# Optimization experiments

Hardware: AMD Instinct MI355X
Metric: run time of the kernel (lower is better)

Reference implementation:

```python
import jax, jax.numpy as jnp
import numpy as np

N_NODES = 50000
N_EDGES = 640000
DIMS = [128, 256, 128]


def setup_inputs() -> dict:
    key = jax.random.key(0)
    ks = jax.random.split(key, 8)
    x = jax.random.normal(ks[0], (N_NODES, DIMS[0]), dtype=jnp.float32)
    src = jax.random.randint(ks[1], (N_EDGES,), 0, N_NODES)
    dst = jax.random.randint(ks[2], (N_EDGES,), 0, N_NODES)
    # ensure no pre-existing self loops so add_remaining_self_loops == append all loops
    dst = jnp.where(dst == src, (dst + 1) % N_NODES, dst)
    edge_index = jnp.stack([src, dst]).astype(jnp.int64)
    # SAGEConv lin_l weights (root_weight=False -> only neighbor linear), Kaiming-ish init
    def lin(k, fan_in, fan_out):
        s = 1.0 / np.sqrt(fan_in)
        kw, kb = jax.random.split(k)
        W = jax.random.uniform(kw, (fan_out, fan_in), minval=-s, maxval=s, dtype=jnp.float32)
        b = jax.random.uniform(kb, (fan_out,), minval=-s, maxval=s, dtype=jnp.float32)
        return W, b
    W1, b1 = lin(ks[3], DIMS[0], DIMS[1])
    W2, b2 = lin(ks[4], DIMS[1], DIMS[2])
    logit_scale = jnp.asarray(np.log(1.0 / 0.07), dtype=jnp.float32)
    return {"x": x, "edge_index": edge_index, "W1": W1, "b1": b1,
            "W2": W2, "b2": b2, "logit_scale": logit_scale}


def reference(x, edge_index, W1, b1, W2, b2, logit_scale):
    N = x.shape[0]
    loops = jnp.arange(N, dtype=edge_index.dtype)
    src = jnp.concatenate([edge_index[0], loops])  # add_remaining_self_loops
    dst = jnp.concatenate([edge_index[1], loops])
    deg = jax.ops.segment_sum(jnp.ones_like(dst, dtype=x.dtype), dst, num_segments=N)
    inv_deg = 1.0 / deg  # deg >= 1 thanks to self loops

    def sage_conv(y, W, b):
        # mean aggregation of source features at destination, then linear
        agg = jax.ops.segment_sum(y[src], dst, num_segments=N) * inv_deg[:, None]
        return agg @ W.T + b

    y = jax.nn.relu(sage_conv(x, W1, b1))
    y = sage_conv(y, W2, b2)
    # F.normalize(p=2, dim=-1, eps=1e-12)
    nrm = jnp.maximum(jnp.linalg.norm(y, axis=-1, keepdims=True), 1e-12)
    y = y / nrm
    return y * jnp.exp(logit_scale)
```

## Files before the change

kernel.cpp:

```cpp
#include <hip/hip_runtime.h>
#include <hip/hip_bf16.h>

#define N_NODES 50000
#define NPAD 50048
#define ZROW N_NODES
#define D0 128
#define D1 256
#define D2 128
#define N4 1600000
#define NB4 1601536
#define CAP 64
#define PREP_BLOCKS 2048

typedef __attribute__((ext_vector_type(8))) short short8;
typedef __attribute__((ext_vector_type(8))) unsigned short ushort8;
typedef __attribute__((ext_vector_type(4))) float f32x4;

static __device__ __forceinline__ unsigned short f2bf(float f) {
    __hip_bfloat16 h = __float2bfloat16(f);
    return *(unsigned short*)&h;
}
static __device__ __forceinline__ float bf2f(unsigned short u) {
    return __uint_as_float(((unsigned int)u) << 16);
}

__global__ __launch_bounds__(256) void k_prep(const float* __restrict__ x,
                                              unsigned short* __restrict__ x_bf,
                                              const float* __restrict__ W1,
                                              const float* __restrict__ W2,
                                              unsigned short* __restrict__ W1p,
                                              unsigned short* __restrict__ W2p,
                                              const int* __restrict__ ei,
                                              int* __restrict__ cursor,
                                              unsigned short* __restrict__ csr, int E) {
    __shared__ int s_is64;
    if (threadIdx.x < 64) {
        int lane = threadIdx.x;
        int nz = 0;
#pragma unroll
        for (int k = 0; k < 4; k++) nz += (ei[2 * (lane * 4 + k) + 1] != 0);
#pragma unroll
        for (int off = 32; off > 0; off >>= 1) nz += __shfl_down(nz, off, 64);
        if (lane == 0) s_is64 = (nz == 0) ? 1 : 0;
    }
    __syncthreads();
    const int NT = PREP_BLOCKS * 256;
    int tid0 = blockIdx.x * 256 + threadIdx.x;

    int npairs = (E + 1) / 2;
    if (tid0 < npairs) {
        int p = tid0;
        int is64 = s_is64;
        int es0, ed0, es1, ed1;
        if (is64) {
            int4 sp = ((const int4*)ei)[p];
            int4 dp = ((const int4*)(ei + 2 * (size_t)E))[p];
            es0 = sp.x; es1 = sp.z; ed0 = dp.x; ed1 = dp.z;
        } else {
            int2 sp = ((const int2*)ei)[p];
            int2 dp = ((const int2*)(ei + (size_t)E))[p];
            es0 = sp.x; es1 = sp.y; ed0 = dp.x; ed1 = dp.y;
        }
        int p0 = atomicAdd(&cursor[ed0], 1);
        if (p0 < CAP) csr[(size_t)ed0 * CAP + p0] = (unsigned short)es0;
        if (2 * p + 1 < E) {
            int p1 = atomicAdd(&cursor[ed1], 1);
            if (p1 < CAP) csr[(size_t)ed1 * CAP + p1] = (unsigned short)es1;
        }
    }

    for (int i = tid0; i < NB4; i += NT) {
        if (i < N4) {
            float4 v = ((const float4*)x)[i];
            ushort4 u;
            u.x = f2bf(v.x); u.y = f2bf(v.y); u.z = f2bf(v.z); u.w = f2bf(v.w);
            ((ushort4*)x_bf)[i] = u;
        } else {
            ushort4 z = {0, 0, 0, 0};
            ((ushort4*)x_bf)[i] = z;
        }
    }

    if (tid0 < 2 * D0 * D1) {
        int idx = tid0;
        if (idx < D0 * D1) {
            int j = idx & 7, lane = (idx >> 3) & 63, tile = idx >> 9;
            int ct = tile & 15, kt = tile >> 4;
            int k = kt * 32 + (lane >> 4) * 8 + j;
            int n = ct * 16 + (lane & 15);
            W1p[idx] = f2bf(W1[n * D0 + k]);
        } else {
            int i2 = idx - D0 * D1;
            int j = i2 & 7, lane = (i2 >> 3) & 63, tile = i2 >> 9;
            int ct = tile & 7, kt = tile >> 3;
            int k = kt * 32 + (lane >> 4) * 8 + j;
            int n = ct * 16 + (lane & 15);
            W2p[i2] = f2bf(W2[n * D1 + k]);
        }
    }
}

#define A_LD 132
#define H_LD 260
__global__ __launch_bounds__(256, 6) void k_gmlp(const unsigned short* __restrict__ x_bf,
                                                 const unsigned short* __restrict__ csr,
                                                 const int* __restrict__ cursor,
                                                 const unsigned short* __restrict__ W1p,
                                                 const float* __restrict__ b1,
                                                 const unsigned short* __restrict__ W2p,
                                                 unsigned short* __restrict__ t_bf) {
    __shared__ unsigned short Abuf[16 * A_LD];
    __shared__ unsigned short Hbuf[16 * H_LD];
    int tid = threadIdx.x;
    int n0 = blockIdx.x * 16;

    {
        int g = tid >> 4, h = tid & 15;
        int node = n0 + g;
        unsigned short* lp = Abuf + g * A_LD + h * 8;
        if (node < N_NODES) {
            int dg = cursor[node]; if (dg > CAP) dg = CAP;
            const unsigned short* cp = csr + (size_t)node * CAP;
            ushort8 u = *(const ushort8*)(x_bf + (size_t)node * 128 + h * 8);
            ushort8 c0 = ((const ushort8*)cp)[0];
            ushort8 c1 = ((const ushort8*)cp)[1];
            int idx[16];
#pragma unroll
            for (int u8 = 0; u8 < 8; u8++) { idx[u8] = c0[u8]; idx[8 + u8] = c1[u8]; }
#pragma unroll
            for (int u8 = 0; u8 < 16; u8++)
                if (u8 >= dg) idx[u8] = ZROW;
            ushort8 rr[16];
#pragma unroll
            for (int u8 = 0; u8 < 16; u8++)
                rr[u8] = *(const ushort8*)(x_bf + (size_t)idx[u8] * 128 + h * 8);
            float a0[8], a1[8];
#pragma unroll
            for (int t = 0; t < 8; t++) { a0[t] = bf2f(u[t]); a1[t] = 0.f; }
#pragma unroll
            for (int t = 0; t < 8; t++) {
                a0[t] += bf2f(rr[0][t]) + bf2f(rr[2][t]) + bf2f(rr[4][t]) + bf2f(rr[6][t])
                       + bf2f(rr[8][t]) + bf2f(rr[10][t]) + bf2f(rr[12][t]) + bf2f(rr[14][t]);
                a1[t] += bf2f(rr[1][t]) + bf2f(rr[3][t]) + bf2f(rr[5][t]) + bf2f(rr[7][t])
                       + bf2f(rr[9][t]) + bf2f(rr[11][t]) + bf2f(rr[13][t]) + bf2f(rr[15][t]);
            }
            for (int j = 16; j < dg; j += 8) {
                int idx2[8];
#pragma unroll
                for (int u8 = 0; u8 < 8; u8++) {
                    int jj = j + u8;
                    idx2[u8] = (jj < dg) ? (int)cp[jj] : ZROW;
                }
                ushort8 r2[8];
#pragma unroll
                for (int u8 = 0; u8 < 8; u8++)
                    r2[u8] = *(const ushort8*)(x_bf + (size_t)idx2[u8] * 128 + h * 8);
#pragma unroll
                for (int t = 0; t < 8; t++) {
                    a0[t] += bf2f(r2[0][t]) + bf2f(r2[2][t]) + bf2f(r2[4][t]) + bf2f(r2[6][t]);
                    a1[t] += bf2f(r2[1][t]) + bf2f(r2[3][t]) + bf2f(r2[5][t]) + bf2f(r2[7][t]);
                }
            }
            float invd = 1.0f / (float)(dg + 1);
            ushort8 o;
#pragma unroll
            for (int t = 0; t < 8; t++) o[t] = f2bf((a0[t] + a1[t]) * invd);
            *(ushort8*)lp = o;
        } else {
            ushort8 z = {0, 0, 0, 0, 0, 0, 0, 0};
            *(ushort8*)lp = z;
        }
    }
    __syncthreads();

    int w = tid >> 6, lane = tid & 63;
    int m = lane & 15, q = lane >> 4;

    {
        short8 af[4];
        const unsigned short* arow = Abuf + m * A_LD + q * 8;
#pragma unroll
        for (int kt = 0; kt < 4; kt++) af[kt] = *(const short8*)(arow + kt * 32);
#pragma unroll
        for (int c = 0; c < 4; c++) {
            int ct = w * 4 + c;
            f32x4 acc = {0.f, 0.f, 0.f, 0.f};
#pragma unroll
            for (int kt = 0; kt < 4; kt++) {
                short8 bw = *(const short8*)(W1p + (((kt * 16 + ct) * 64 + lane) << 3));
                acc = __builtin_amdgcn_mfma_f32_16x16x32_bf16(af[kt], bw, acc, 0, 0, 0);
            }
            int col = ct * 16 + m;
            float bias = b1[col];
#pragma unroll
            for (int r = 0; r < 4; r++)
                Hbuf[(q * 4 + r) * H_LD + col] = f2bf(fmaxf(acc[r] + bias, 0.0f));
        }
    }
    __syncthreads();

    {
        short8 hf[8];
        const unsigned short* hrow = Hbuf + m * H_LD + q * 8;
#pragma unroll
        for (int kt = 0; kt < 8; kt++) hf[kt] = *(const short8*)(hrow + kt * 32);
#pragma unroll
        for (int c = 0; c < 2; c++) {
            int ct = w * 2 + c;
            f32x4 acc = {0.f, 0.f, 0.f, 0.f};
#pragma unroll
            for (int kt = 0; kt < 8; kt++) {
                short8 bw = *(const short8*)(W2p + (((kt * 8 + ct) * 64 + lane) << 3));
                acc = __builtin_amdgcn_mfma_f32_16x16x32_bf16(hf[kt], bw, acc, 0, 0, 0);
            }
            int col = ct * 16 + m;
#pragma unroll
            for (int r = 0; r < 4; r++) {
                int node = n0 + q * 4 + r;
                t_bf[(size_t)node * 128 + col] = (node < N_NODES) ? f2bf(acc[r]) : (unsigned short)0;
            }
        }
    }
}

__global__ __launch_bounds__(256) void k_gather_final(const unsigned short* __restrict__ t,
                                                      const unsigned short* __restrict__ csr,
                                                      const int* __restrict__ cursor,
                                                      const float* __restrict__ b2,
                                                      const float* __restrict__ ls,
                                                      float* __restrict__ out) {
    int tid = threadIdx.x;
    int h = tid & 15;
    int node = blockIdx.x * 16 + (tid >> 4);

    int dg = cursor[node]; if (dg > CAP) dg = CAP;
    const unsigned short* cp = csr + (size_t)node * CAP;
    ushort8 u = *(const ushort8*)(t + (size_t)node * 128 + h * 8);
    ushort8 c0 = ((const ushort8*)cp)[0];
    ushort8 c1 = ((const ushort8*)cp)[1];
    int idx[16];
#pragma unroll
    for (int u8 = 0; u8 < 8; u8++) { idx[u8] = c0[u8]; idx[8 + u8] = c1[u8]; }
#pragma unroll
    for (int u8 = 0; u8 < 16; u8++)
        if (u8 >= dg) idx[u8] = ZROW;
    ushort8 rr[16];
#pragma unroll
    for (int u8 = 0; u8 < 16; u8++)
        rr[u8] = *(const ushort8*)(t + (size_t)idx[u8] * 128 + h * 8);
    float a0[8], a1[8];
#pragma unroll
    for (int k = 0; k < 8; k++) { a0[k] = bf2f(u[k]); a1[k] = 0.f; }
#pragma unroll
    for (int k = 0; k < 8; k++) {
        a0[k] += bf2f(rr[0][k]) + bf2f(rr[2][k]) + bf2f(rr[4][k]) + bf2f(rr[6][k])
               + bf2f(rr[8][k]) + bf2f(rr[10][k]) + bf2f(rr[12][k]) + bf2f(rr[14][k]);
        a1[k] += bf2f(rr[1][k]) + bf2f(rr[3][k]) + bf2f(rr[5][k]) + bf2f(rr[7][k])
               + bf2f(rr[9][k]) + bf2f(rr[11][k]) + bf2f(rr[13][k]) + bf2f(rr[15][k]);
    }
    for (int j = 16; j < dg; j += 8) {
        int idx2[8];
#pragma unroll
        for (int u8 = 0; u8 < 8; u8++) {
            int jj = j + u8;
            idx2[u8] = (jj < dg) ? (int)cp[jj] : ZROW;
        }
        ushort8 r2[8];
#pragma unroll
        for (int u8 = 0; u8 < 8; u8++)
            r2[u8] = *(const ushort8*)(t + (size_t)idx2[u8] * 128 + h * 8);
#pragma unroll
        for (int k = 0; k < 8; k++) {
            a0[k] += bf2f(r2[0][k]) + bf2f(r2[2][k]) + bf2f(r2[4][k]) + bf2f(r2[6][k]);
            a1[k] += bf2f(r2[1][k]) + bf2f(r2[3][k]) + bf2f(r2[5][k]) + bf2f(r2[7][k]);
        }
    }
    float invd = 1.0f / (float)(dg + 1);
    float4 bb0 = ((const float4*)b2)[h * 2];
    float4 bb1 = ((const float4*)b2)[h * 2 + 1];
    float v[8];
    v[0] = (a0[0] + a1[0]) * invd + bb0.x;
    v[1] = (a0[1] + a1[1]) * invd + bb0.y;
    v[2] = (a0[2] + a1[2]) * invd + bb0.z;
    v[3] = (a0[3] + a1[3]) * invd + bb0.w;
    v[4] = (a0[4] + a1[4]) * invd + bb1.x;
    v[5] = (a0[5] + a1[5]) * invd + bb1.y;
    v[6] = (a0[6] + a1[6]) * invd + bb1.z;
    v[7] = (a0[7] + a1[7]) * invd + bb1.w;

    float s = 0.f;
#pragma unroll
    for (int k = 0; k < 8; k++) s += v[k] * v[k];
#pragma unroll
    for (int msk = 8; msk > 0; msk >>= 1) s += __shfl_xor(s, msk, 64);
    float nrm = fmaxf(sqrtf(s), 1e-12f);
    float scale = expf(ls[0]) / nrm;
    float4 o0, o1;
    o0.x = v[0] * scale; o0.y = v[1] * scale; o0.z = v[2] * scale; o0.w = v[3] * scale;
    o1.x = v[4] * scale; o1.y = v[5] * scale; o1.z = v[6] * scale; o1.w = v[7] * scale;
    float* op = out + (size_t)node * 128 + h * 8;
    *(float4*)(op + 0) = o0;
    *(float4*)(op + 4) = o1;
}

extern "C" void kernel_launch(void* const* d_in, const int* in_sizes, int n_in,
                              void* d_out, int out_size, void* d_ws, size_t ws_size,
                              hipStream_t stream) {
    const float* x  = (const float*)d_in[0];
    const int*   ei = (const int*)d_in[1];
    const float* W1 = (const float*)d_in[2];
    const float* b1 = (const float*)d_in[3];
    const float* W2 = (const float*)d_in[4];
    const float* b2 = (const float*)d_in[5];
    const float* ls = (const float*)d_in[6];
    float* out = (float*)d_out;

    const int E = in_sizes[1] / 2;

    char* ws = (char*)d_ws;
    size_t off = 0;
    auto alloc = [&](size_t bytes) {
        size_t o = off;
        off = (off + bytes + 255) & ~(size_t)255;
        return o;
    };
    int*            cursor = (int*)(ws + alloc((size_t)N_NODES * 4));
    unsigned short* csr    = (unsigned short*)(ws + alloc((size_t)N_NODES * CAP * 2));
    unsigned short* W1p    = (unsigned short*)(ws + alloc((size_t)D0 * D1 * 2));
    unsigned short* W2p    = (unsigned short*)(ws + alloc((size_t)D1 * D2 * 2));
    unsigned short* x_bf   = (unsigned short*)(ws + alloc((size_t)NPAD * D0 * 2));
    unsigned short* t_bf   = (unsigned short*)(ws + alloc((size_t)NPAD * D2 * 2));

    hipMemsetAsync(cursor, 0, (size_t)N_NODES * 4, stream);
    k_prep<<<PREP_BLOCKS, 256, 0, stream>>>(x, x_bf, W1, W2, W1p, W2p, ei, cursor, csr, E);
    k_gmlp<<<NPAD / 16, 256, 0, stream>>>(x_bf, csr, cursor, W1p, b1, W2p, t_bf);
    k_gather_final<<<N_NODES / 16, 256, 0, stream>>>(t_bf, csr, cursor, b2, ls, out);
}
```

Before: 191.7 us.

## Partition CSR build per XCD with workgroup-scope atomics and a compaction pass

Edge-to-CSR insertion now gives each of the 8 XCDs its own cursor array and slot region, so the atomics can use workgroup scope and stay in the local L2 instead of contending at device scope. A new compaction kernel merges the per-XCD slot lists into the original fixed-capacity CSR. This costs an extra kernel launch, a memset eight times larger and more memory traffic. Correctness relies on the hardware register read identifying the XCD and on per-XCD L2 coherence holding with workgroup-scope atomics, which is a subtle memory-model risk.

```diff
diff --git a/kernel.cpp b/kernel.cpp
--- a/kernel.cpp
+++ b/kernel.cpp
@@ -10,6 +10,8 @@
 #define N4 1600000
 #define NB4 1601536
 #define CAP 64
+#define CAP8 32
+#define NXCD 8
 #define PREP_BLOCKS 2048
 
 typedef __attribute__((ext_vector_type(8))) short short8;
@@ -22,6 +24,12 @@
 }
 static __device__ __forceinline__ float bf2f(unsigned short u) {
     return __uint_as_float(((unsigned int)u) << 16);
+}
+
+static __device__ __forceinline__ int get_xcc() {
+    unsigned x;
+    asm volatile("s_getreg_b32 %0, hwreg(20, 0, 32)" : "=s"(x));
+    return (int)(x & (NXCD - 1));
 }
 
 __global__ __launch_bounds__(256) void k_prep(const float* __restrict__ x,
@@ -31,8 +39,8 @@
                                               unsigned short* __restrict__ W1p,
                                               unsigned short* __restrict__ W2p,
                                               const int* __restrict__ ei,
-                                              int* __restrict__ cursor,
-                                              unsigned short* __restrict__ csr, int E) {
+                                              int* __restrict__ cursor8,
+                                              unsigned short* __restrict__ csr8, int E) {
     __shared__ int s_is64;
     if (threadIdx.x < 64) {
         int lane = threadIdx.x;
@@ -49,6 +57,7 @@
 
     int npairs = (E + 1) / 2;
     if (tid0 < npairs) {
+        int xcc = get_xcc();
         int p = tid0;
         int is64 = s_is64;
         int es0, ed0, es1, ed1;
@@ -61,11 +70,15 @@
             int2 dp = ((const int2*)(ei + (size_t)E))[p];
             es0 = sp.x; es1 = sp.y; ed0 = dp.x; ed1 = dp.y;
         }
-        int p0 = atomicAdd(&cursor[ed0], 1);
-        if (p0 < CAP) csr[(size_t)ed0 * CAP + p0] = (unsigned short)es0;
+        int p0 = __hip_atomic_fetch_add(&cursor8[xcc * N_NODES + ed0], 1,
+                                        __ATOMIC_RELAXED, __HIP_MEMORY_SCOPE_WORKGROUP);
+        if (p0 < CAP8)
+            csr8[(size_t)ed0 * (NXCD * CAP8) + xcc * CAP8 + p0] = (unsigned short)es0;
         if (2 * p + 1 < E) {
-            int p1 = atomicAdd(&cursor[ed1], 1);
-            if (p1 < CAP) csr[(size_t)ed1 * CAP + p1] = (unsigned short)es1;
+            int p1 = __hip_atomic_fetch_add(&cursor8[xcc * N_NODES + ed1], 1,
+                                            __ATOMIC_RELAXED, __HIP_MEMORY_SCOPE_WORKGROUP);
+            if (p1 < CAP8)
+                csr8[(size_t)ed1 * (NXCD * CAP8) + xcc * CAP8 + p1] = (unsigned short)es1;
         }
     }
 
@@ -100,6 +113,38 @@
     }
 }
 
+__global__ __launch_bounds__(256) void k_compact(const int* __restrict__ cursor8,
+                                                 const unsigned short* __restrict__ csr8,
+                                                 int* __restrict__ cursor,
+                                                 unsigned short* __restrict__ csr) {
+    int node = blockIdx.x * 256 + threadIdx.x;
+    if (node >= N_NODES) return;
+    const unsigned short* src = csr8 + (size_t)node * (NXCD * CAP8);
+    unsigned short* dstp = csr + (size_t)node * CAP;
+    int c[NXCD];
+#pragma unroll
+    for (int s = 0; s < NXCD; s++) {
+        int cs = cursor8[s * N_NODES + node];
+        c[s] = (cs > CAP8) ? CAP8 : cs;
+    }
+    ushort4 iv[NXCD];
+#pragma unroll
+    for (int s = 0; s < NXCD; s++) iv[s] = *(const ushort4*)(src + s * CAP8);
+    int off = 0;
+#pragma unroll
+    for (int s = 0; s < NXCD; s++) {
+        int cs = c[s];
+        if (cs > 0 && off + 0 < CAP) dstp[off + 0] = iv[s].x;
+        if (cs > 1 && off + 1 < CAP) dstp[off + 1] = iv[s].y;
+        if (cs > 2 && off + 2 < CAP) dstp[off + 2] = iv[s].z;
+        if (cs > 3 && off + 3 < CAP) dstp[off + 3] = iv[s].w;
+        for (int k = 4; k < cs; k++)
+            if (off + k < CAP) dstp[off + k] = src[s * CAP8 + k];
+        off += cs;
+    }
+    cursor[node] = off;
+}
+
 #define A_LD 132
 #define H_LD 260
 __global__ __launch_bounds__(256, 6) void k_gmlp(const unsigned short* __restrict__ x_bf,
@@ -324,15 +369,18 @@
         off = (off + bytes + 255) & ~(size_t)255;
         return o;
     };
-    int*            cursor = (int*)(ws + alloc((size_t)N_NODES * 4));
-    unsigned short* csr    = (unsigned short*)(ws + alloc((size_t)N_NODES * CAP * 2));
-    unsigned short* W1p    = (unsigned short*)(ws + alloc((size_t)D0 * D1 * 2));
-    unsigned short* W2p    = (unsigned short*)(ws + alloc((size_t)D1 * D2 * 2));
-    unsigned short* x_bf   = (unsigned short*)(ws + alloc((size_t)NPAD * D0 * 2));
-    unsigned short* t_bf   = (unsigned short*)(ws + alloc((size_t)NPAD * D2 * 2));
-
-    hipMemsetAsync(cursor, 0, (size_t)N_NODES * 4, stream);
-    k_prep<<<PREP_BLOCKS, 256, 0, stream>>>(x, x_bf, W1, W2, W1p, W2p, ei, cursor, csr, E);
+    int*            cursor8 = (int*)(ws + alloc((size_t)NXCD * N_NODES * 4));
+    unsigned short* csr8    = (unsigned short*)(ws + alloc((size_t)N_NODES * NXCD * CAP8 * 2));
+    int*            cursor  = (int*)(ws + alloc((size_t)N_NODES * 4));
+    unsigned short* csr     = (unsigned short*)(ws + alloc((size_t)N_NODES * CAP * 2));
+    unsigned short* W1p     = (unsigned short*)(ws + alloc((size_t)D0 * D1 * 2));
+    unsigned short* W2p     = (unsigned short*)(ws + alloc((size_t)D1 * D2 * 2));
+    unsigned short* x_bf    = (unsigned short*)(ws + alloc((size_t)NPAD * D0 * 2));
+    unsigned short* t_bf    = (unsigned short*)(ws + alloc((size_t)NPAD * D2 * 2));
+
+    hipMemsetAsync(cursor8, 0, (size_t)NXCD * N_NODES * 4, stream);
+    k_prep<<<PREP_BLOCKS, 256, 0, stream>>>(x, x_bf, W1, W2, W1p, W2p, ei, cursor8, csr8, E);
+    k_compact<<<(N_NODES + 255) / 256, 256, 0, stream>>>(cursor8, csr8, cursor, csr);
     k_gmlp<<<NPAD / 16, 256, 0, stream>>>(x_bf, csr, cursor, W1p, b1, W2p, t_bf);
     k_gather_final<<<N_NODES / 16, 256, 0, stream>>>(t_bf, csr, cursor, b2, ls, out);
 }
```

Result: slower. 200.5 us (+4.6%).
